# Performance work log

Measured on AMD Instinct MI355X. Metric: run time of the kernel, lower is better.

The kernel has to match this reference:

```python
import jax, jax.numpy as jnp
import numpy as np

R, S, D, V, K, B, L, U, I = 20000, 64, 128, 50000, 32, 2048, 20480, 100000, 100000


def setup_inputs() -> dict:
    key = jax.random.key(0)
    ks = jax.random.split(key, 16)
    # segment ids: equal-sized history per batch element (guaranteed non-empty)
    seg = (jnp.arange(L, dtype=jnp.int32) // (L // B)).astype(jnp.int32)
    return {
        "user": jax.random.randint(ks[0], (B,), 0, U, dtype=jnp.int32),
        "item": jax.random.randint(ks[1], (B,), 0, I, dtype=jnp.int32),
        "historical_review": jax.random.randint(ks[2], (R, S), 0, V, dtype=jnp.int32),
        "historical_review_positive": jax.random.normal(ks[3], (R, D), jnp.float32),
        "user_hist_idx": jax.random.randint(ks[4], (L,), 0, R, dtype=jnp.int32),
        "user_hist_seg": seg,
        "item_hist_idx": jax.random.randint(ks[5], (L,), 0, R, dtype=jnp.int32),
        "item_hist_seg": seg,
        "word_emb": jax.random.normal(ks[6], (V, D), jnp.float32) * 0.02,
        "M_w": jax.random.normal(ks[7], (D, D), jnp.float32) * (1.0 / np.sqrt(D)),
        "M_b": jnp.zeros((D,), jnp.float32),
        "W_w": jax.random.normal(ks[8], (D, K), jnp.float32) * (1.0 / np.sqrt(D)),
        "W_b": jnp.zeros((K,), jnp.float32),
        "T_w": jax.random.normal(ks[9], (K, D), jnp.float32) * (1.0 / np.sqrt(K)),
        "T_b": jnp.zeros((D,), jnp.float32),
        "user_emb": jax.random.normal(ks[10], (U, D), jnp.float32) * 0.02,
        "item_emb": jax.random.normal(ks[11], (I, D), jnp.float32) * 0.02,
        "avg_rating": jnp.full((1,), 3.5, jnp.float32),
    }


def _segment_mean(x, seg, num_segments):
    s = jax.ops.segment_sum(x, seg, num_segments=num_segments)
    c = jax.ops.segment_sum(jnp.ones(seg.shape, x.dtype), seg, num_segments=num_segments)
    return s / jnp.maximum(c, 1.0)[:, None]


def reference(user, item, historical_review, historical_review_positive,
              user_hist_idx, user_hist_seg, item_hist_idx, item_hist_seg,
              word_emb, M_w, M_b, W_w, W_b, T_w, T_b,
              user_emb, item_emb, avg_rating):
    # --- aspect extraction (ABAE-style) over R historical reviews ---
    e_w = word_emb[historical_review]                      # [R, S, D] gather
    y_s = historical_review_positive                       # [R, D] sentence embedding
    # dx = transform_M(e_w) @ y_s  -> attention logits over words
    dx = jnp.einsum('rsd,de,re->rs', e_w, M_w, y_s) + jnp.einsum('d,rd->r', M_b, y_s)[:, None]
    ax = jax.nn.softmax(dx, axis=1)                        # [R, S]
    z_s = jnp.einsum('rsd,rs->rd', e_w, ax)                # [R, D]
    p_t = jax.nn.softmax(z_s @ W_w + W_b, axis=1)          # [R, K] aspect probs
    r_s = p_t @ T_w + T_b                                  # [R, D] aspect-based review embedding
    # --- ragged gather + mean-pool over user/item histories ---
    ua = _segment_mean(r_s[user_hist_idx], user_hist_seg, B)  # [B, D]
    ia = _segment_mean(r_s[item_hist_idx], item_hist_seg, B)  # [B, D]
    uf = user_emb[user]                                    # [B, D]
    itf = item_emb[item]                                   # [B, D]
    prediction = jnp.sum(ua * ia, axis=-1) + jnp.sum(uf * itf, axis=-1) + avg_rating[0]
    return prediction  # [B]
```

## Files before the change

kernel.cpp:

```cpp
#include <hip/hip_runtime.h>


typedef __attribute__((ext_vector_type(8))) short bf16x8;
typedef __attribute__((ext_vector_type(4))) float f32x4;

__device__ __forceinline__ unsigned int f2bf_rne(float x) {
  unsigned int u = __float_as_uint(x);
  return (u + 0x7fffu + ((u >> 16) & 1u)) >> 16;
}
__device__ __forceinline__ float bf_lo(unsigned int w) { return __uint_as_float(w << 16); }
__device__ __forceinline__ float bf_hi(unsigned int w) { return __uint_as_float(w & 0xffff0000u); }

__global__ __launch_bounds__(256) void kA_mfma(
    const float* __restrict__ We, const float* __restrict__ Mw,
    const float* __restrict__ Ww, unsigned char* __restrict__ Z, int V) {
  __shared__ uint4 Bs[2560];
  int t = threadIdx.x;
  int L = t & 63, wid = t >> 6;

#pragma unroll
  for (int q = 0; q < 10; ++q) {
    int c = t + q * 256;
    int cl = c & 63, g = c >> 6;
    int jt = g >> 2, ks = g & 3;
    int n = jt * 16 + (cl & 15);
    int k0 = ks * 32 + (cl >> 4) * 8;
    float v[8];
#pragma unroll
    for (int j = 0; j < 8; ++j) {
      int e = k0 + j;
      v[j] = (n < 128) ? Mw[(size_t)e * 128 + n] : Ww[(size_t)e * 32 + (n - 128)];
    }
    uint4 pk;
    pk.x = f2bf_rne(v[0]) | (f2bf_rne(v[1]) << 16);
    pk.y = f2bf_rne(v[2]) | (f2bf_rne(v[3]) << 16);
    pk.z = f2bf_rne(v[4]) | (f2bf_rne(v[5]) << 16);
    pk.w = f2bf_rne(v[6]) | (f2bf_rne(v[7]) << 16);
    Bs[c] = pk;
  }
  __syncthreads();

  int r0 = blockIdx.x * 64;
  if (r0 > V - 64) r0 = V - 64;
  int rowA = r0 + wid * 16 + (L & 15);
  const float4* Arow = (const float4*)(We + (size_t)rowA * 128);

  f32x4 acc[10];
#pragma unroll
  for (int jt = 0; jt < 10; ++jt) acc[jt] = (f32x4){0.f, 0.f, 0.f, 0.f};

#pragma unroll
  for (int ks = 0; ks < 4; ++ks) {
    int koff4 = ks * 8 + (L >> 4) * 2;
    float4 a0 = Arow[koff4];
    float4 a1 = Arow[koff4 + 1];
    union { uint4 u; bf16x8 v; } A;
    A.u.x = f2bf_rne(a0.x) | (f2bf_rne(a0.y) << 16);
    A.u.y = f2bf_rne(a0.z) | (f2bf_rne(a0.w) << 16);
    A.u.z = f2bf_rne(a1.x) | (f2bf_rne(a1.y) << 16);
    A.u.w = f2bf_rne(a1.z) | (f2bf_rne(a1.w) << 16);
#pragma unroll
    for (int jt = 0; jt < 10; ++jt) {
      union { uint4 u; bf16x8 v; } Bf;
      Bf.u = Bs[(jt * 4 + ks) * 64 + L];
      acc[jt] = __builtin_amdgcn_mfma_f32_16x16x32_bf16(A.v, Bf.v, acc[jt], 0, 0, 0);
    }
  }

#pragma unroll
  for (int jt = 0; jt < 10; ++jt) {
#pragma unroll
    for (int i = 0; i < 4; ++i) {
      unsigned int u = f2bf_rne(acc[jt][i]);
      unsigned int partner = (unsigned int)__shfl_xor((int)u, 1);
      if (!(L & 1)) {
        int col = jt * 16 + (L & 15);
        int orow = r0 + wid * 16 + (L >> 4) * 4 + i;
        *(unsigned int*)(Z + (size_t)orow * 320 + col * 2) = u | (partner << 16);
      }
    }
  }
}

__global__ __launch_bounds__(256) void k3_review(
    const int* __restrict__ hr, const float* __restrict__ Y,
    const unsigned char* __restrict__ Z, const float* __restrict__ Wb,
    const float* __restrict__ Tw, const float* __restrict__ Tb,
    float* __restrict__ rs, int R) {
  __shared__ int hr_s[4][64];
  __shared__ __align__(16) float y_s[4][128];
  __shared__ float dx_s[4][64];
  __shared__ float ax_s[4][64];
  __shared__ float p_s[4][32];
  int t = threadIdx.x;
  int w = t >> 6, lane = t & 63;
  int r = blockIdx.x * 4 + w;
  if (r >= R) r = R - 1;

  hr_s[w][lane] = hr[(size_t)r * 64 + lane];
  ((float2*)y_s[w])[lane] = ((const float2*)Y)[(size_t)r * 64 + lane];
  __syncthreads();

  int g = lane & 15, sub = lane >> 4;
  const float4* y4 = (const float4*)y_s[w];
  const unsigned char* bp[4];
#pragma unroll
  for (int p = 0; p < 4; ++p) {
    int wid = hr_s[w][p * 16 + g];
    bp[p] = Z + (size_t)wid * 320 + sub * 16;
  }
  float dxp[4];
#pragma unroll
  for (int p = 0; p < 4; ++p) {
    float acc = 0.f;
#pragma unroll
    for (int i = 0; i < 4; ++i) {
      uint4 q = *(const uint4*)(bp[p] + i * 64);
      float4 ya = y4[i * 8 + sub * 2];
      float4 yb = y4[i * 8 + sub * 2 + 1];
      acc += bf_lo(q.x) * ya.x + bf_hi(q.x) * ya.y
           + bf_lo(q.y) * ya.z + bf_hi(q.y) * ya.w
           + bf_lo(q.z) * yb.x + bf_hi(q.z) * yb.y
           + bf_lo(q.w) * yb.z + bf_hi(q.w) * yb.w;
    }
    acc += __shfl_xor(acc, 16);
    acc += __shfl_xor(acc, 32);
    dxp[p] = acc;
  }
  if (sub == 0) {
#pragma unroll
    for (int p = 0; p < 4; ++p) dx_s[w][p * 16 + g] = dxp[p];
  }
  __syncthreads();

  float dx = dx_s[w][lane];
  float m = dx;
#pragma unroll
  for (int off = 32; off; off >>= 1) m = fmaxf(m, __shfl_xor(m, off));
  float ex = __expf(dx - m);
  float sum = ex;
#pragma unroll
  for (int off = 32; off; off >>= 1) sum += __shfl_xor(sum, off);
  ax_s[w][lane] = ex / sum;
  __syncthreads();

  int k = lane & 31, half = lane >> 5;
  float lg = 0.f;
#pragma unroll 8
  for (int j = 0; j < 32; ++j) {
    int s = half * 32 + j;
    int wid = hr_s[w][s];
    unsigned short u = *(const unsigned short*)(Z + (size_t)wid * 320 + 256 + k * 2);
    lg += ax_s[w][s] * __uint_as_float(((unsigned int)u) << 16);
  }
  lg += __shfl_xor(lg, 32);
  lg += Wb[k];
  float mk = lg;
#pragma unroll
  for (int off = 16; off; off >>= 1) mk = fmaxf(mk, __shfl_xor(mk, off));
  float ek = __expf(lg - mk);
  float sk = ek;
#pragma unroll
  for (int off = 16; off; off >>= 1) sk += __shfl_xor(sk, off);
  if (half == 0) p_s[w][k] = ek / sk;
  __syncthreads();

  const float2* T2 = (const float2*)Tw;
  float2 acc = ((const float2*)Tb)[lane];
#pragma unroll 8
  for (int kk = 0; kk < 32; ++kk) {
    float pk = p_s[w][kk];
    float2 tv = T2[kk * 64 + lane];
    acc.x += pk * tv.x;
    acc.y += pk * tv.y;
  }
  ((float2*)rs)[(size_t)r * 64 + lane] = acc;
}

__global__ __launch_bounds__(256) void k4_final(
    const float* __restrict__ rs, const int* __restrict__ uidx,
    const int* __restrict__ iidx, const int* __restrict__ user,
    const int* __restrict__ item, const float* __restrict__ uemb,
    const float* __restrict__ iemb, const float* __restrict__ avg,
    float* __restrict__ out, int B, int per) {
  int t = threadIdx.x;
  int w = t >> 6, lane = t & 63;
  int b = blockIdx.x * 4 + w;
  if (b >= B) return;
  const float2* rs2 = (const float2*)rs;
  float2 ua = {0.f, 0.f}, ia = {0.f, 0.f};
  int base = b * per;
  for (int j = 0; j < per; ++j) {
    int id = uidx[base + j];
    float2 tv = rs2[(size_t)id * 64 + lane];
    ua.x += tv.x; ua.y += tv.y;
  }
  for (int j = 0; j < per; ++j) {
    int id = iidx[base + j];
    float2 tv = rs2[(size_t)id * 64 + lane];
    ia.x += tv.x; ia.y += tv.y;
  }
  float inv = 1.0f / (float)per;
  float part = (ua.x * ia.x + ua.y * ia.y) * inv * inv;
  float2 uf = ((const float2*)uemb)[(size_t)user[b] * 64 + lane];
  float2 itf = ((const float2*)iemb)[(size_t)item[b] * 64 + lane];
  part += uf.x * itf.x + uf.y * itf.y;
#pragma unroll
  for (int off = 32; off; off >>= 1) part += __shfl_xor(part, off);
  if (lane == 0) out[b] = part + avg[0];
}

extern "C" void kernel_launch(void* const* d_in, const int* in_sizes, int n_in,
                              void* d_out, int out_size, void* d_ws, size_t ws_size,
                              hipStream_t stream) {
  const int*   user = (const int*)d_in[0];
  const int*   item = (const int*)d_in[1];
  const int*   hr   = (const int*)d_in[2];
  const float* Y    = (const float*)d_in[3];
  const int*   uhi  = (const int*)d_in[4];
  const int*   ihi  = (const int*)d_in[6];
  const float* We   = (const float*)d_in[8];
  const float* Mw   = (const float*)d_in[9];
  const float* Ww   = (const float*)d_in[11];
  const float* Wb   = (const float*)d_in[12];
  const float* Tw   = (const float*)d_in[13];
  const float* Tb   = (const float*)d_in[14];
  const float* Ue   = (const float*)d_in[15];
  const float* Ie   = (const float*)d_in[16];
  const float* avg  = (const float*)d_in[17];

  int B = in_sizes[0];
  int R = in_sizes[3] / 128;
  int V = in_sizes[8] / 128;
  int L = in_sizes[4];
  int per = L / B;

  unsigned char* Z = (unsigned char*)d_ws;
  float* rsbuf = (float*)(Z + (size_t)V * 320);
  float* out = (float*)d_out;

  kA_mfma<<<(V + 63) / 64, 256, 0, stream>>>(We, Mw, Ww, Z, V);
  k3_review<<<(R + 3) / 4, 256, 0, stream>>>(hr, Y, Z, Wb, Tw, Tb, rsbuf, R);
  k4_final<<<(B + 3) / 4, 256, 0, stream>>>(rsbuf, uhi, ihi, user, item, Ue, Ie, avg, out, B, per);
}
```

Before: 259.5 us.

## Store projected word table in fp8 and use shuffles instead of LDS in review kernel

The projected word table (word_emb @ M_w) is now stored as scaled fp8 instead of bf16, with the W_w part kept in bf16. This shrinks each row from 320 to 192 bytes and cuts the gather traffic in the review kernel. The review kernel drops its shared-memory staging and barriers and uses wave shuffles for word ids, attention weights and aspect probabilities. The projection kernel becomes a grid-stride loop with a third as many blocks, amortising the per-block weight staging. fp8 quantisation of the attention logits risks accuracy loss.

```diff
diff --git a/kernel.cpp b/kernel.cpp
--- a/kernel.cpp
+++ b/kernel.cpp
@@ -3,17 +3,17 @@
 
 typedef __attribute__((ext_vector_type(8))) short bf16x8;
 typedef __attribute__((ext_vector_type(4))) float f32x4;
+typedef __attribute__((ext_vector_type(2))) float vf2;
 
 __device__ __forceinline__ unsigned int f2bf_rne(float x) {
   unsigned int u = __float_as_uint(x);
   return (u + 0x7fffu + ((u >> 16) & 1u)) >> 16;
 }
-__device__ __forceinline__ float bf_lo(unsigned int w) { return __uint_as_float(w << 16); }
-__device__ __forceinline__ float bf_hi(unsigned int w) { return __uint_as_float(w & 0xffff0000u); }
 
 __global__ __launch_bounds__(256) void kA_mfma(
     const float* __restrict__ We, const float* __restrict__ Mw,
-    const float* __restrict__ Ww, unsigned char* __restrict__ Z, int V) {
+    const float* __restrict__ Ww, unsigned char* __restrict__ Z,
+    int V, int ntiles) {
   __shared__ uint4 Bs[2560];
   int t = threadIdx.x;
   int L = t & 63, wid = t >> 6;
@@ -40,46 +40,78 @@
   }
   __syncthreads();
 
-  int r0 = blockIdx.x * 64;
-  if (r0 > V - 64) r0 = V - 64;
-  int rowA = r0 + wid * 16 + (L & 15);
-  const float4* Arow = (const float4*)(We + (size_t)rowA * 128);
-
-  f32x4 acc[10];
-#pragma unroll
-  for (int jt = 0; jt < 10; ++jt) acc[jt] = (f32x4){0.f, 0.f, 0.f, 0.f};
-
-#pragma unroll
-  for (int ks = 0; ks < 4; ++ks) {
-    int koff4 = ks * 8 + (L >> 4) * 2;
-    float4 a0 = Arow[koff4];
-    float4 a1 = Arow[koff4 + 1];
-    union { uint4 u; bf16x8 v; } A;
-    A.u.x = f2bf_rne(a0.x) | (f2bf_rne(a0.y) << 16);
-    A.u.y = f2bf_rne(a0.z) | (f2bf_rne(a0.w) << 16);
-    A.u.z = f2bf_rne(a1.x) | (f2bf_rne(a1.y) << 16);
-    A.u.w = f2bf_rne(a1.z) | (f2bf_rne(a1.w) << 16);
-#pragma unroll
-    for (int jt = 0; jt < 10; ++jt) {
-      union { uint4 u; bf16x8 v; } Bf;
-      Bf.u = Bs[(jt * 4 + ks) * 64 + L];
-      acc[jt] = __builtin_amdgcn_mfma_f32_16x16x32_bf16(A.v, Bf.v, acc[jt], 0, 0, 0);
-    }
-  }
-
-#pragma unroll
-  for (int jt = 0; jt < 10; ++jt) {
-#pragma unroll
-    for (int i = 0; i < 4; ++i) {
-      unsigned int u = f2bf_rne(acc[jt][i]);
-      unsigned int partner = (unsigned int)__shfl_xor((int)u, 1);
-      if (!(L & 1)) {
-        int col = jt * 16 + (L & 15);
-        int orow = r0 + wid * 16 + (L >> 4) * 4 + i;
-        *(unsigned int*)(Z + (size_t)orow * 320 + col * 2) = u | (partner << 16);
+  for (int tile = blockIdx.x; tile < ntiles; tile += gridDim.x) {
+    int r0 = tile * 64;
+    if (r0 > V - 64) r0 = V - 64;
+    int rowA = r0 + wid * 16 + (L & 15);
+    const float4* Arow = (const float4*)(We + (size_t)rowA * 128);
+
+    f32x4 acc[10];
+#pragma unroll
+    for (int jt = 0; jt < 10; ++jt) acc[jt] = (f32x4){0.f, 0.f, 0.f, 0.f};
+
+#pragma unroll
+    for (int ks = 0; ks < 4; ++ks) {
+      int koff4 = ks * 8 + (L >> 4) * 2;
+      float4 a0 = Arow[koff4];
+      float4 a1 = Arow[koff4 + 1];
+      union { uint4 u; bf16x8 v; } A;
+      A.u.x = f2bf_rne(a0.x) | (f2bf_rne(a0.y) << 16);
+      A.u.y = f2bf_rne(a0.z) | (f2bf_rne(a0.w) << 16);
+      A.u.z = f2bf_rne(a1.x) | (f2bf_rne(a1.y) << 16);
+      A.u.w = f2bf_rne(a1.z) | (f2bf_rne(a1.w) << 16);
+#pragma unroll
+      for (int jt = 0; jt < 10; ++jt) {
+        union { uint4 u; bf16x8 v; } Bf;
+        Bf.u = Bs[(jt * 4 + ks) * 64 + L];
+        acc[jt] = __builtin_amdgcn_mfma_f32_16x16x32_bf16(A.v, Bf.v, acc[jt], 0, 0, 0);
       }
     }
-  }
+
+#pragma unroll
+    for (int jt = 0; jt < 8; ++jt) {
+#pragma unroll
+      for (int i = 0; i < 4; ++i) {
+        float v0 = acc[jt][i] * 64.f;
+        float v1 = __shfl_xor(v0, 1);
+        float v2 = __shfl_xor(v0, 2);
+        float v3 = __shfl_xor(v0, 3);
+        if (!(L & 3)) {
+          int col = jt * 16 + (L & 15);
+          int orow = r0 + wid * 16 + (L >> 4) * 4 + i;
+          int w8 = __builtin_amdgcn_cvt_pk_fp8_f32(v0, v1, 0, false);
+          w8 = __builtin_amdgcn_cvt_pk_fp8_f32(v2, v3, w8, true);
+          *(int*)(Z + (size_t)orow * 192 + col) = w8;
+        }
+      }
+    }
+#pragma unroll
+    for (int jt = 8; jt < 10; ++jt) {
+#pragma unroll
+      for (int i = 0; i < 4; ++i) {
+        unsigned int u = f2bf_rne(acc[jt][i]);
+        unsigned int partner = (unsigned int)__shfl_xor((int)u, 1);
+        if (!(L & 1)) {
+          int k = (jt - 8) * 16 + (L & 15);
+          int orow = r0 + wid * 16 + (L >> 4) * 4 + i;
+          *(unsigned int*)(Z + (size_t)orow * 192 + 128 + k * 2) = u | (partner << 16);
+        }
+      }
+    }
+  }
+}
+
+__device__ __forceinline__ float dot_fp8_16(uint4 q, const float4* y) {
+  float s = 0.f;
+#pragma unroll
+  for (int i = 0; i < 4; ++i) {
+    unsigned int u = (&q.x)[i];
+    vf2 a = __builtin_amdgcn_cvt_pk_f32_fp8(u, false);
+    vf2 b = __builtin_amdgcn_cvt_pk_f32_fp8(u, true);
+    float4 yv = y[i];
+    s += a.x * yv.x + a.y * yv.y + b.x * yv.z + b.y * yv.w;
+  }
+  return s;
 }
 
 __global__ __launch_bounds__(256) void k3_review(
@@ -87,53 +119,47 @@
     const unsigned char* __restrict__ Z, const float* __restrict__ Wb,
     const float* __restrict__ Tw, const float* __restrict__ Tb,
     float* __restrict__ rs, int R) {
-  __shared__ int hr_s[4][64];
-  __shared__ __align__(16) float y_s[4][128];
-  __shared__ float dx_s[4][64];
-  __shared__ float ax_s[4][64];
-  __shared__ float p_s[4][32];
   int t = threadIdx.x;
-  int w = t >> 6, lane = t & 63;
-  int r = blockIdx.x * 4 + w;
+  int wv = t >> 6, lane = t & 63;
+  int r = blockIdx.x * 4 + wv;
   if (r >= R) r = R - 1;
 
-  hr_s[w][lane] = hr[(size_t)r * 64 + lane];
-  ((float2*)y_s[w])[lane] = ((const float2*)Y)[(size_t)r * 64 + lane];
-  __syncthreads();
-
+  int word = hr[(size_t)r * 64 + lane];
   int g = lane & 15, sub = lane >> 4;
-  const float4* y4 = (const float4*)y_s[w];
+
+  const float4* Yr = (const float4*)(Y + (size_t)r * 128);
+  float4 ya[4], yb[4];
+#pragma unroll
+  for (int i = 0; i < 4; ++i) {
+    ya[i] = Yr[sub * 4 + i];
+    yb[i] = Yr[16 + sub * 4 + i];
+  }
+
   const unsigned char* bp[4];
 #pragma unroll
   for (int p = 0; p < 4; ++p) {
-    int wid = hr_s[w][p * 16 + g];
-    bp[p] = Z + (size_t)wid * 320 + sub * 16;
+    int wid = __shfl(word, p * 16 + g);
+    bp[p] = Z + (size_t)wid * 192 + sub * 16;
+  }
+  uint4 q0[4], q1[4];
+#pragma unroll
+  for (int p = 0; p < 4; ++p) {
+    q0[p] = *(const uint4*)(bp[p]);
+    q1[p] = *(const uint4*)(bp[p] + 64);
   }
   float dxp[4];
 #pragma unroll
   for (int p = 0; p < 4; ++p) {
-    float acc = 0.f;
-#pragma unroll
-    for (int i = 0; i < 4; ++i) {
-      uint4 q = *(const uint4*)(bp[p] + i * 64);
-      float4 ya = y4[i * 8 + sub * 2];
-      float4 yb = y4[i * 8 + sub * 2 + 1];
-      acc += bf_lo(q.x) * ya.x + bf_hi(q.x) * ya.y
-           + bf_lo(q.y) * ya.z + bf_hi(q.y) * ya.w
-           + bf_lo(q.z) * yb.x + bf_hi(q.z) * yb.y
-           + bf_lo(q.w) * yb.z + bf_hi(q.w) * yb.w;
-    }
+    float acc = dot_fp8_16(q0[p], ya) + dot_fp8_16(q1[p], yb);
     acc += __shfl_xor(acc, 16);
     acc += __shfl_xor(acc, 32);
-    dxp[p] = acc;
-  }
-  if (sub == 0) {
-#pragma unroll
-    for (int p = 0; p < 4; ++p) dx_s[w][p * 16 + g] = dxp[p];
-  }
-  __syncthreads();
-
-  float dx = dx_s[w][lane];
+    dxp[p] = acc * 0.015625f;
+  }
+  float dx = dxp[0];
+  dx = (sub == 1) ? dxp[1] : dx;
+  dx = (sub == 2) ? dxp[2] : dx;
+  dx = (sub == 3) ? dxp[3] : dx;
+
   float m = dx;
 #pragma unroll
   for (int off = 32; off; off >>= 1) m = fmaxf(m, __shfl_xor(m, off));
@@ -141,17 +167,17 @@
   float sum = ex;
 #pragma unroll
   for (int off = 32; off; off >>= 1) sum += __shfl_xor(sum, off);
-  ax_s[w][lane] = ex / sum;
-  __syncthreads();
+  float ax = ex / sum;
 
   int k = lane & 31, half = lane >> 5;
   float lg = 0.f;
 #pragma unroll 8
   for (int j = 0; j < 32; ++j) {
     int s = half * 32 + j;
-    int wid = hr_s[w][s];
-    unsigned short u = *(const unsigned short*)(Z + (size_t)wid * 320 + 256 + k * 2);
-    lg += ax_s[w][s] * __uint_as_float(((unsigned int)u) << 16);
+    int wid_s = __shfl(word, s);
+    float ax_s = __shfl(ax, s);
+    unsigned short u = *(const unsigned short*)(Z + (size_t)wid_s * 192 + 128 + k * 2);
+    lg += ax_s * __uint_as_float(((unsigned int)u) << 16);
   }
   lg += __shfl_xor(lg, 32);
   lg += Wb[k];
@@ -162,19 +188,18 @@
   float sk = ek;
 #pragma unroll
   for (int off = 16; off; off >>= 1) sk += __shfl_xor(sk, off);
-  if (half == 0) p_s[w][k] = ek / sk;
-  __syncthreads();
+  float p_own = ek / sk;
 
   const float2* T2 = (const float2*)Tw;
-  float2 acc = ((const float2*)Tb)[lane];
+  float2 acc2 = ((const float2*)Tb)[lane];
 #pragma unroll 8
   for (int kk = 0; kk < 32; ++kk) {
-    float pk = p_s[w][kk];
+    float pk = __shfl(p_own, kk);
     float2 tv = T2[kk * 64 + lane];
-    acc.x += pk * tv.x;
-    acc.y += pk * tv.y;
-  }
-  ((float2*)rs)[(size_t)r * 64 + lane] = acc;
+    acc2.x += pk * tv.x;
+    acc2.y += pk * tv.y;
+  }
+  ((float2*)rs)[(size_t)r * 64 + lane] = acc2;
 }
 
 __global__ __launch_bounds__(256) void k4_final(
@@ -236,10 +261,12 @@
   int per = L / B;
 
   unsigned char* Z = (unsigned char*)d_ws;
-  float* rsbuf = (float*)(Z + (size_t)V * 320);
+  float* rsbuf = (float*)(Z + (size_t)V * 192);
   float* out = (float*)d_out;
 
-  kA_mfma<<<(V + 63) / 64, 256, 0, stream>>>(We, Mw, Ww, Z, V);
+  int ntiles = (V + 63) / 64;
+  int ka_grid = (ntiles + 2) / 3;
+  kA_mfma<<<ka_grid, 256, 0, stream>>>(We, Mw, Ww, Z, V, ntiles);
   k3_review<<<(R + 3) / 4, 256, 0, stream>>>(hr, Y, Z, Wb, Tw, Tb, rsbuf, R);
   k4_final<<<(B + 3) / 4, 256, 0, stream>>>(rsbuf, uhi, ihi, user, item, Ue, Ie, avg, out, B, per);
 }
```

Result: faster. 254.2 us (-2.0%).
